# Kernel tuning notes

Hardware: AMD Instinct MI355X
Metric: run time of the kernel (lower is better)

Reference implementation:

```python
import jax, jax.numpy as jnp
from jax import lax
import numpy as np

B, CIN, L = 16, 512, 1024
COUT, K = 1024, 5          # conv out channels (GLU halves to 512), kernel size
DW = 512                    # word_feat == attn_channels == img_conv channels
HW = 196                    # 14*14 image feature locations


def setup_inputs() -> dict:
    key = jax.random.key(0)
    ks = jax.random.split(key, 8)
    s = 0.02
    return {
        "x": jax.random.normal(ks[0], (B, CIN, L), jnp.float32),
        "word_embed": jax.random.normal(ks[1], (B, L, DW), jnp.float32),
        "img_conv": jax.random.normal(ks[2], (B, DW, 14, 14), jnp.float32),
        "prev_attn": jnp.zeros((B, L, HW), jnp.float32),  # passed through, unused
        "conv_v": jax.random.normal(ks[3], (COUT, CIN, K), jnp.float32) * s,
        "conv_g": jnp.ones((COUT,), jnp.float32),
        "conv_b": jnp.zeros((COUT,), jnp.float32),
        "fc1_w": jax.random.normal(ks[4], (DW, DW), jnp.float32) * s,
        "fc1_b": jnp.zeros((DW,), jnp.float32),
        "fc2_w": jax.random.normal(ks[5], (DW, DW), jnp.float32) * s,
        "fc2_b": jnp.zeros((DW,), jnp.float32),
    }


def reference(x, word_embed, img_conv, prev_attn,
              conv_v, conv_g, conv_b, fc1_w, fc1_b, fc2_w, fc2_b):
    k = conv_v.shape[-1]
    # weight norm (PyTorch default dim=0): w = g * v / ||v||_{(in,k)}
    v_norm = jnp.sqrt(jnp.sum(conv_v * conv_v, axis=(1, 2), keepdims=True))
    w = (conv_g[:, None, None] / v_norm) * conv_v
    # Conv1d, padding=k-1 on both sides -> length L + k - 1 after ConvS2S trim
    y = lax.conv_general_dilated(x, w, window_strides=(1,),
                                 padding=[(k - 1, k - 1)],
                                 dimension_numbers=("NCH", "OIH", "NCH"))
    y = y + conv_b[None, :, None]
    # dropout is identity in eval mode
    a, b = jnp.split(y, 2, axis=1)          # GLU over channel dim
    h = a * jax.nn.sigmoid(b)
    h = h[:, :, : -(k - 1)]                  # [B, DW, L]
    identity_attn = h
    # attn_fc1 on [B, L, DW] then add word embeddings
    q = jnp.einsum("bcl,ac->bla", h, fc1_w) + fc1_b + word_embed  # [B, L, DW]
    feat = img_conv.reshape(img_conv.shape[0], img_conv.shape[1], -1)  # [B, DW, HW]
    score = jnp.einsum("bla,bap->blp", q, feat)   # [B, L, HW]
    attn = jax.nn.softmax(score, axis=-1)         # softmax over image locations
    ctx = jnp.einsum("blp,bap->bla", attn, feat)  # [B, L, DW]
    o = jnp.einsum("bla,ca->blc", ctx, fc2_w) + fc2_b
    out = o.transpose(0, 2, 1) + identity_attn
    # identity.shape == out.shape (input_feat == output_feat/2) -> no downsample
    out = out + x
    return (out, word_embed, img_conv, attn)
```

## Files before the change

### kernel.cpp

```cpp
#include <hip/hip_runtime.h>
#include <math.h>

#define NB   16
#define NCIN 512
#define NL   1024
#define NCOUT 1024
#define NK   5
#define NDW  512
#define NHW  196
#define NP   208
#define NPK  224

typedef unsigned short ushort_t;
typedef unsigned int uint_t;
typedef __attribute__((ext_vector_type(8))) short bf16x8;
typedef __attribute__((ext_vector_type(4))) float f32x4;

static __device__ __forceinline__ ushort_t f2bf(float f) {
  uint_t u = __builtin_bit_cast(uint_t, f);
  u += 0x7fff + ((u >> 16) & 1);
  return (ushort_t)(u >> 16);
}
static __device__ __forceinline__ float bf2f(ushort_t u) {
  uint_t v = ((uint_t)u) << 16;
  return __builtin_bit_cast(float, v);
}

__global__ __launch_bounds__(256) void wnorm_kernel(
    const float* __restrict__ v, const float* __restrict__ g,
    ushort_t* __restrict__ wperm) {
  const int o = blockIdx.x;
  const float* vr = v + (size_t)o * (NCIN * NK);
  float s = 0.f;
  for (int j = threadIdx.x; j < NCIN * NK; j += 256) {
    float t = vr[j];
    s += t * t;
  }
  for (int off = 32; off; off >>= 1) s += __shfl_down(s, off, 64);
  __shared__ float red[4];
  __shared__ float scale_s;
  const int wid = threadIdx.x >> 6;
  if ((threadIdx.x & 63) == 0) red[wid] = s;
  __syncthreads();
  if (threadIdx.x == 0) {
    float tot = red[0] + red[1] + red[2] + red[3];
    scale_s = g[o] / sqrtf(tot);
  }
  __syncthreads();
  const float scale = scale_s;
#pragma unroll
  for (int dk = 0; dk < NK; ++dk) {
    for (int ci = threadIdx.x; ci < NCIN; ci += 256) {
      wperm[((size_t)dk * NCOUT + o) * NCIN + ci] = f2bf(vr[ci * NK + dk] * scale);
    }
  }
}

__global__ __launch_bounds__(256) void xpose_kernel(
    const float* __restrict__ x, ushort_t* __restrict__ xT) {
  const int b = blockIdx.z;
  const int ci0 = blockIdx.y * 64;
  const int l0 = blockIdx.x * 64;
  const int tid = threadIdx.x;
  __shared__ float t[64][65];
  const float* xb = x + ((size_t)b * NCIN + ci0) * NL + l0;
#pragma unroll
  for (int r = 0; r < 4; ++r) {
    int row = r * 16 + (tid >> 4);
    int col = (tid & 15) * 4;
    float4 v = *(const float4*)&xb[(size_t)row * NL + col];
    t[row][col + 0] = v.x; t[row][col + 1] = v.y;
    t[row][col + 2] = v.z; t[row][col + 3] = v.w;
  }
  __syncthreads();
  ushort_t* xo = xT + ((size_t)b * NL + l0) * NCIN + ci0;
#pragma unroll
  for (int r = 0; r < 4; ++r) {
    int lrow = r * 16 + (tid >> 4);
    int cic = (tid & 15) * 4;
    ushort4 o4;
    o4.x = f2bf(t[cic + 0][lrow]);
    o4.y = f2bf(t[cic + 1][lrow]);
    o4.z = f2bf(t[cic + 2][lrow]);
    o4.w = f2bf(t[cic + 3][lrow]);
    *(ushort4*)&xo[(size_t)lrow * NCIN + cic] = o4;
  }
}

__global__ __launch_bounds__(256) void wcvt_kernel(
    const float* __restrict__ w1, const float* __restrict__ w2,
    ushort_t* __restrict__ w1bf, ushort_t* __restrict__ w2bf) {
  const int i = (blockIdx.x * 256 + threadIdx.x) * 4;
  {
    float4 v = *(const float4*)&w1[i];
    ushort4 o; o.x = f2bf(v.x); o.y = f2bf(v.y); o.z = f2bf(v.z); o.w = f2bf(v.w);
    *(ushort4*)&w1bf[i] = o;
  }
  {
    float4 v = *(const float4*)&w2[i];
    ushort4 o; o.x = f2bf(v.x); o.y = f2bf(v.y); o.z = f2bf(v.z); o.w = f2bf(v.w);
    *(ushort4*)&w2bf[i] = o;
  }
}

__global__ __launch_bounds__(256) void ftrans_kernel(
    const float* __restrict__ feat, ushort_t* __restrict__ fThi,
    ushort_t* __restrict__ fTlo, ushort_t* __restrict__ fbf) {
  const int b = blockIdx.y;
  const int a0 = blockIdx.x * 64;
  const int tid = threadIdx.x;
  __shared__ float t[64][200];

  const float* fb_ = feat + ((size_t)b * NDW + a0) * NHW;
#pragma unroll
  for (int pp = 0; pp < 16; ++pp) {
    int row = pp * 4 + (tid >> 6);
#pragma unroll
    for (int cc = 0; cc < 4; ++cc) {
      int col = cc * 64 + (tid & 63);
      if (col < NHW) t[row][col] = fb_[(size_t)row * NHW + col];
    }
  }
  __syncthreads();

  for (int pp = 0; pp < 13; ++pp) {
    int p = pp * 16 + (tid >> 4);
    int j = (tid & 15) * 4;
    ushort4 hi4, lo4;
#pragma unroll
    for (int k = 0; k < 4; ++k) {
      float v = (p < NHW) ? t[j + k][p] : 0.f;
      ushort_t h = f2bf(v);
      float lof = v - bf2f(h);
      ushort_t l = f2bf(lof);
      ((ushort_t*)&hi4)[k] = h;
      ((ushort_t*)&lo4)[k] = l;
    }
    size_t base = ((size_t)b * NP + p) * NDW + a0 + j;
    *(ushort4*)&fThi[base] = hi4;
    *(ushort4*)&fTlo[base] = lo4;
  }

#pragma unroll
  for (int cc = 0; cc < 4; ++cc) {
    int col = cc * 64 + (tid & 63);
    if (col < NPK) {
#pragma unroll
      for (int rr = 0; rr < 16; ++rr) {
        int al = rr * 4 + (tid >> 6);
        float v = (col < NHW) ? t[al][col] : 0.f;
        fbf[((size_t)b * NDW + a0 + al) * NPK + col] = f2bf(v);
      }
    }
  }
}

__global__ __launch_bounds__(256, 2) void conv_glu_mfma(
    const ushort_t* __restrict__ xT, const ushort_t* __restrict__ wperm,
    const float* __restrict__ conv_b, ushort_t* __restrict__ hbfT) {
  const int b  = blockIdx.z;
  const int c0 = blockIdx.y * 128;
  const int l0 = blockIdx.x * 128;
  const int tid = threadIdx.x;
  const int wid = tid >> 6;
  const int lane = tid & 63;
  const int wl = wid & 1;
  const int wc = wid >> 1;
  const int quad = lane >> 4;
  const int l16 = lane & 15;

  __shared__ ushort_t lx[128][72];
  __shared__ ushort_t lw[256][72];

  f32x4 accA[4][4], accB[4][4];
#pragma unroll
  for (int mt = 0; mt < 4; ++mt)
#pragma unroll
    for (int nt = 0; nt < 4; ++nt) {
      accA[mt][nt] = (f32x4){0.f, 0.f, 0.f, 0.f};
      accB[mt][nt] = (f32x4){0.f, 0.f, 0.f, 0.f};
    }

  const ushort_t* xTb = xT + (size_t)b * NL * NCIN;

  for (int dk = 0; dk < NK; ++dk) {
    const int lbase = l0 + dk - 4;
    const ushort_t* wpb = wperm + (size_t)dk * NCOUT * NCIN;
    for (int ci0 = 0; ci0 < NCIN; ci0 += 64) {
      __syncthreads();
#pragma unroll
      for (int it = 0; it < 4; ++it) {
        int t = tid + it * 256;
        int r = t >> 3, seg = t & 7;
        int gl = lbase + r;
        uint4 v = make_uint4(0u, 0u, 0u, 0u);
        if (gl >= 0)
          v = *(const uint4*)(xTb + (size_t)gl * NCIN + ci0 + seg * 8);
        *(uint4*)&lx[r][seg * 8] = v;
      }
#pragma unroll
      for (int it = 0; it < 8; ++it) {
        int t = tid + it * 256;
        int r = t >> 3, seg = t & 7;
        int co = (it < 4) ? (c0 + r) : (384 + c0 + r);
        uint4 v = *(const uint4*)(wpb + (size_t)co * NCIN + ci0 + seg * 8);
        *(uint4*)&lw[r][seg * 8] = v;
      }
      __syncthreads();
#pragma unroll
      for (int ks = 0; ks < 2; ++ks) {
        bf16x8 af[4];
#pragma unroll
        for (int mt = 0; mt < 4; ++mt)
          af[mt] = *(const bf16x8*)&lx[wl * 64 + mt * 16 + l16][ks * 32 + quad * 8];
#pragma unroll
        for (int nt = 0; nt < 4; ++nt) {
          bf16x8 bfa = *(const bf16x8*)&lw[wc * 64 + nt * 16 + l16][ks * 32 + quad * 8];
          bf16x8 bfb = *(const bf16x8*)&lw[128 + wc * 64 + nt * 16 + l16][ks * 32 + quad * 8];
#pragma unroll
          for (int mt = 0; mt < 4; ++mt) {
            accA[mt][nt] = __builtin_amdgcn_mfma_f32_16x16x32_bf16(af[mt], bfa, accA[mt][nt], 0, 0, 0);
            accB[mt][nt] = __builtin_amdgcn_mfma_f32_16x16x32_bf16(af[mt], bfb, accB[mt][nt], 0, 0, 0);
          }
        }
      }
    }
  }

#pragma unroll
  for (int nt = 0; nt < 4; ++nt) {
    const int co = c0 + wc * 64 + nt * 16 + l16;
    const float ba = conv_b[co];
    const float bb = conv_b[co + 512];
#pragma unroll
    for (int mt = 0; mt < 4; ++mt) {
      const int l = l0 + wl * 64 + mt * 16 + quad * 4;
      f32x4 a4 = accA[mt][nt];
      f32x4 b4 = accB[mt][nt];
#pragma unroll
      for (int r = 0; r < 4; ++r) {
        float aa = a4[r] + ba, bg = b4[r] + bb;
        float hv = aa * (1.f / (1.f + __expf(-bg)));
        hbfT[((size_t)b * NL + l + r) * NDW + co] = f2bf(hv);
      }
    }
  }
}

__global__ __launch_bounds__(256, 2) void fc1_mfma(
    const ushort_t* __restrict__ hbfT, const ushort_t* __restrict__ w1bf,
    const float* __restrict__ fb, const float* __restrict__ we,
    ushort_t* __restrict__ qhi, ushort_t* __restrict__ qlo) {
  const int b  = blockIdx.z;
  const int a0 = blockIdx.y * 128;
  const int l0 = blockIdx.x * 128;
  const int tid = threadIdx.x;
  const int wid = tid >> 6;
  const int lane = tid & 63;
  const int wl = wid & 1;
  const int wc = wid >> 1;
  const int quad = lane >> 4;
  const int l16 = lane & 15;

  __shared__ ushort_t la[128][72];
  __shared__ ushort_t lb[128][72];

  f32x4 acc[4][4];
#pragma unroll
  for (int mt = 0; mt < 4; ++mt)
#pragma unroll
    for (int nt = 0; nt < 4; ++nt) acc[mt][nt] = (f32x4){0.f, 0.f, 0.f, 0.f};

  const ushort_t* hb = hbfT + (size_t)b * NL * NDW;

  for (int c0 = 0; c0 < NDW; c0 += 64) {
    __syncthreads();
#pragma unroll
    for (int it = 0; it < 4; ++it) {
      int t = tid + it * 256;
      int r = t >> 3, seg = t & 7;
      *(uint4*)&la[r][seg * 8] = *(const uint4*)(hb + (size_t)(l0 + r) * NDW + c0 + seg * 8);
    }
#pragma unroll
    for (int it = 0; it < 4; ++it) {
      int t = tid + it * 256;
      int r = t >> 3, seg = t & 7;
      *(uint4*)&lb[r][seg * 8] = *(const uint4*)(w1bf + (size_t)(a0 + r) * NDW + c0 + seg * 8);
    }
    __syncthreads();
#pragma unroll
    for (int ks = 0; ks < 2; ++ks) {
      bf16x8 af[4];
#pragma unroll
      for (int mt = 0; mt < 4; ++mt)
        af[mt] = *(const bf16x8*)&la[wl * 64 + mt * 16 + l16][ks * 32 + quad * 8];
#pragma unroll
      for (int nt = 0; nt < 4; ++nt) {
        bf16x8 bf = *(const bf16x8*)&lb[wc * 64 + nt * 16 + l16][ks * 32 + quad * 8];
#pragma unroll
        for (int mt = 0; mt < 4; ++mt)
          acc[mt][nt] = __builtin_amdgcn_mfma_f32_16x16x32_bf16(af[mt], bf, acc[mt][nt], 0, 0, 0);
      }
    }
  }

#pragma unroll
  for (int nt = 0; nt < 4; ++nt) {
    const int a = a0 + wc * 64 + nt * 16 + l16;
    const float bias = fb[a];
#pragma unroll
    for (int mt = 0; mt < 4; ++mt) {
      const int l = l0 + wl * 64 + mt * 16 + quad * 4;
#pragma unroll
      for (int r = 0; r < 4; ++r) {
        size_t idx = ((size_t)b * NL + l + r) * NDW + a;
        float qv = acc[mt][nt][r] + bias + we[idx];
        ushort_t h = f2bf(qv);
        float lof = qv - bf2f(h);
        qhi[idx] = h;
        qlo[idx] = f2bf(lof);
      }
    }
  }
}

__global__ __launch_bounds__(256) void score_softmax(
    const ushort_t* __restrict__ qhi, const ushort_t* __restrict__ qlo,
    const ushort_t* __restrict__ fThi, const ushort_t* __restrict__ fTlo,
    float* __restrict__ out_attn) {
  const int b  = blockIdx.y;
  const int l0 = blockIdx.x * 64;
  const int tid = threadIdx.x;
  const int wid = tid >> 6;
  const int lane = tid & 63;
  const int quad = lane >> 4;
  const int l16 = lane & 15;

  __shared__ ushort_t qh[64][36], ql[64][36];
  __shared__ ushort_t fh[208][36], fl[208][36];

  f32x4 acc[13];
#pragma unroll
  for (int nt = 0; nt < 13; ++nt) acc[nt] = (f32x4){0.f, 0.f, 0.f, 0.f};

  for (int kc = 0; kc < 16; ++kc) {
    const int a0 = kc * 32;
    __syncthreads();
    {
      int r = tid >> 2, seg = tid & 3;
      size_t src = ((size_t)b * NL + l0 + r) * NDW + a0 + seg * 8;
      *(uint4*)&qh[r][seg * 8] = *(const uint4*)(qhi + src);
      *(uint4*)&ql[r][seg * 8] = *(const uint4*)(qlo + src);
#pragma unroll
      for (int it = 0; it < 4; ++it) {
        int row = it * 64 + (tid >> 2);
        if (row < NP) {
          size_t fsrc = ((size_t)b * NP + row) * NDW + a0 + seg * 8;
          *(uint4*)&fh[row][seg * 8] = *(const uint4*)(fThi + fsrc);
          *(uint4*)&fl[row][seg * 8] = *(const uint4*)(fTlo + fsrc);
        }
      }
    }
    __syncthreads();
    bf16x8 ah = *(const bf16x8*)&qh[wid * 16 + l16][quad * 8];
    bf16x8 al = *(const bf16x8*)&ql[wid * 16 + l16][quad * 8];
#pragma unroll
    for (int nt = 0; nt < 13; ++nt) {
      bf16x8 bh = *(const bf16x8*)&fh[nt * 16 + l16][quad * 8];
      bf16x8 bl = *(const bf16x8*)&fl[nt * 16 + l16][quad * 8];
      acc[nt] = __builtin_amdgcn_mfma_f32_16x16x32_bf16(ah, bh, acc[nt], 0, 0, 0);
      acc[nt] = __builtin_amdgcn_mfma_f32_16x16x32_bf16(al, bh, acc[nt], 0, 0, 0);
      acc[nt] = __builtin_amdgcn_mfma_f32_16x16x32_bf16(ah, bl, acc[nt], 0, 0, 0);
    }
  }

  const bool v12 = (l16 < 4);
#pragma unroll
  for (int r = 0; r < 4; ++r) {
    float mx = -1e30f;
#pragma unroll
    for (int nt = 0; nt < 12; ++nt) mx = fmaxf(mx, acc[nt][r]);
    if (v12) mx = fmaxf(mx, acc[12][r]);
#pragma unroll
    for (int off = 1; off < 16; off <<= 1) mx = fmaxf(mx, __shfl_xor(mx, off, 16));
    float ex[13];
    float sum = 0.f;
#pragma unroll
    for (int nt = 0; nt < 12; ++nt) { ex[nt] = __expf(acc[nt][r] - mx); sum += ex[nt]; }
    ex[12] = v12 ? __expf(acc[12][r] - mx) : 0.f;
    sum += ex[12];
#pragma unroll
    for (int off = 1; off < 16; off <<= 1) sum += __shfl_xor(sum, off, 16);
    const float inv = 1.f / sum;
    const int l = l0 + wid * 16 + quad * 4 + r;
    float* ao = out_attn + ((size_t)b * NL + l) * NHW;
#pragma unroll
    for (int nt = 0; nt < 13; ++nt) {
      int p = nt * 16 + l16;
      if (p < NHW) ao[p] = ex[nt] * inv;
    }
  }
}

__global__ __launch_bounds__(256, 2) void ctx_mfma(
    const float* __restrict__ attn, const ushort_t* __restrict__ fbf,
    ushort_t* __restrict__ ctx_bf) {
  const int b  = blockIdx.z;
  const int a0 = blockIdx.y * 128;
  const int l0 = blockIdx.x * 128;
  const int tid = threadIdx.x;
  const int wid = tid >> 6;
  const int lane = tid & 63;
  const int wl = wid & 1;
  const int wc = wid >> 1;
  const int quad = lane >> 4;
  const int l16 = lane & 15;

  __shared__ ushort_t la[128][36];
  __shared__ ushort_t lb[128][36];

  f32x4 acc[4][4];
#pragma unroll
  for (int mt = 0; mt < 4; ++mt)
#pragma unroll
    for (int nt = 0; nt < 4; ++nt) acc[mt][nt] = (f32x4){0.f, 0.f, 0.f, 0.f};

  for (int kc = 0; kc < 7; ++kc) {
    const int p0 = kc * 32;
    __syncthreads();
#pragma unroll
    for (int it = 0; it < 2; ++it) {
      int r = it * 64 + (tid >> 2), seg = tid & 3;
      int pb = p0 + seg * 8;
      const float* src = attn + ((size_t)b * NL + l0 + r) * NHW + pb;
      ushort4 o[2];
      if (pb + 7 < NHW) {
        float4 v0 = *(const float4*)src;
        float4 v1 = *(const float4*)(src + 4);
        o[0].x = f2bf(v0.x); o[0].y = f2bf(v0.y); o[0].z = f2bf(v0.z); o[0].w = f2bf(v0.w);
        o[1].x = f2bf(v1.x); o[1].y = f2bf(v1.y); o[1].z = f2bf(v1.z); o[1].w = f2bf(v1.w);
      } else {
#pragma unroll
        for (int k = 0; k < 8; ++k) {
          float v = (pb + k < NHW) ? src[k] : 0.f;
          ((ushort_t*)o)[k] = f2bf(v);
        }
      }
      *(uint4*)&la[r][seg * 8] = *(uint4*)o;
      const ushort_t* fsrc = fbf + ((size_t)b * NDW + a0 + r) * NPK + pb;
      *(uint4*)&lb[r][seg * 8] = *(const uint4*)fsrc;
    }
    __syncthreads();
    bf16x8 af[4];
#pragma unroll
    for (int mt = 0; mt < 4; ++mt)
      af[mt] = *(const bf16x8*)&la[wl * 64 + mt * 16 + l16][quad * 8];
#pragma unroll
    for (int nt = 0; nt < 4; ++nt) {
      bf16x8 bf = *(const bf16x8*)&lb[wc * 64 + nt * 16 + l16][quad * 8];
#pragma unroll
      for (int mt = 0; mt < 4; ++mt)
        acc[mt][nt] = __builtin_amdgcn_mfma_f32_16x16x32_bf16(af[mt], bf, acc[mt][nt], 0, 0, 0);
    }
  }

#pragma unroll
  for (int nt = 0; nt < 4; ++nt) {
    const int a = a0 + wc * 64 + nt * 16 + l16;
#pragma unroll
    for (int mt = 0; mt < 4; ++mt) {
      const int l = l0 + wl * 64 + mt * 16 + quad * 4;
#pragma unroll
      for (int r = 0; r < 4; ++r)
        ctx_bf[((size_t)b * NL + l + r) * NDW + a] = f2bf(acc[mt][nt][r]);
    }
  }
}

__global__ __launch_bounds__(256, 2) void fc2_mfma(
    const ushort_t* __restrict__ w2bf, const ushort_t* __restrict__ ctx_bf,
    const float* __restrict__ fb2, const ushort_t* __restrict__ hbfT,
    const float* __restrict__ x, float* __restrict__ out0) {
  const int b  = blockIdx.z;
  const int c0 = blockIdx.y * 128;
  const int l0 = blockIdx.x * 128;
  const int tid = threadIdx.x;
  const int wid = tid >> 6;
  const int lane = tid & 63;
  const int wl = wid & 1;
  const int wc = wid >> 1;
  const int quad = lane >> 4;
  const int l16 = lane & 15;

  __shared__ ushort_t la[128][72];
  __shared__ ushort_t lb[128][72];

  f32x4 acc[4][4];
#pragma unroll
  for (int mt = 0; mt < 4; ++mt)
#pragma unroll
    for (int nt = 0; nt < 4; ++nt) acc[mt][nt] = (f32x4){0.f, 0.f, 0.f, 0.f};

  for (int a0 = 0; a0 < NDW; a0 += 64) {
    __syncthreads();
#pragma unroll
    for (int it = 0; it < 4; ++it) {
      int t = tid + it * 256;
      int r = t >> 3, seg = t & 7;
      *(uint4*)&la[r][seg * 8] = *(const uint4*)(w2bf + (size_t)(c0 + r) * NDW + a0 + seg * 8);
    }
#pragma unroll
    for (int it = 0; it < 4; ++it) {
      int t = tid + it * 256;
      int r = t >> 3, seg = t & 7;
      *(uint4*)&lb[r][seg * 8] =
          *(const uint4*)(ctx_bf + ((size_t)b * NL + l0 + r) * NDW + a0 + seg * 8);
    }
    __syncthreads();
#pragma unroll
    for (int ks = 0; ks < 2; ++ks) {
      bf16x8 af[4];
#pragma unroll
      for (int mt = 0; mt < 4; ++mt)
        af[mt] = *(const bf16x8*)&la[wl * 64 + mt * 16 + l16][ks * 32 + quad * 8];
#pragma unroll
      for (int nt = 0; nt < 4; ++nt) {
        bf16x8 bf = *(const bf16x8*)&lb[wc * 64 + nt * 16 + l16][ks * 32 + quad * 8];
#pragma unroll
        for (int mt = 0; mt < 4; ++mt)
          acc[mt][nt] = __builtin_amdgcn_mfma_f32_16x16x32_bf16(af[mt], bf, acc[mt][nt], 0, 0, 0);
      }
    }
  }

#pragma unroll
  for (int mt = 0; mt < 4; ++mt) {
    const int cb = c0 + wl * 64 + mt * 16 + quad * 4;
    float4 bias4 = *(const float4*)&fb2[cb];
#pragma unroll
    for (int nt = 0; nt < 4; ++nt) {
      const int l = l0 + wc * 64 + nt * 16 + l16;
      ushort4 h4 = *(const ushort4*)&hbfT[((size_t)b * NL + l) * NDW + cb];
      const float bias[4] = {bias4.x, bias4.y, bias4.z, bias4.w};
      const ushort_t hs[4] = {h4.x, h4.y, h4.z, h4.w};
#pragma unroll
      for (int r = 0; r < 4; ++r) {
        size_t idx = ((size_t)b * NDW + cb + r) * NL + l;
        out0[idx] = acc[mt][nt][r] + bias[r] + bf2f(hs[r]) + x[idx];
      }
    }
  }
}

extern "C" void kernel_launch(void* const* d_in, const int* in_sizes, int n_in,
                              void* d_out, int out_size, void* d_ws, size_t ws_size,
                              hipStream_t stream) {
  const float* x      = (const float*)d_in[0];
  const float* we     = (const float*)d_in[1];
  const float* img    = (const float*)d_in[2];
  const float* conv_v = (const float*)d_in[4];
  const float* conv_g = (const float*)d_in[5];
  const float* conv_b = (const float*)d_in[6];
  const float* fc1_w  = (const float*)d_in[7];
  const float* fc1_b  = (const float*)d_in[8];
  const float* fc2_w  = (const float*)d_in[9];
  const float* fc2_b  = (const float*)d_in[10];

  float* out0     = (float*)d_out;
  float* out_we   = out0 + 8388608;
  float* out_img  = out_we + 8388608;
  float* out_attn = out_img + 1605632;

  ushort_t* wsu = (ushort_t*)d_ws;
  ushort_t* qhi   = wsu;
  ushort_t* qlo   = wsu + 8388608;
  ushort_t* wperm = wsu;
  ushort_t* xT    = wsu + 2621440;
  ushort_t* ctx_b = wsu;
  ushort_t* hbfT  = wsu + 16777216;
  ushort_t* w1bf  = wsu + 25165824;
  ushort_t* w2bf  = wsu + 25428968 - 263144 + 262144 + 144;
  w2bf = wsu + 25165824 + 262144;
  ushort_t* fThi  = wsu + 25690112;
  ushort_t* fTlo  = wsu + 27394048;
  ushort_t* fbf   = wsu + 29097984;

  wnorm_kernel<<<dim3(NCOUT), 256, 0, stream>>>(conv_v, conv_g, wperm);
  xpose_kernel<<<dim3(16, 8, NB), 256, 0, stream>>>(x, xT);
  wcvt_kernel<<<dim3(256), 256, 0, stream>>>(fc1_w, fc2_w, w1bf, w2bf);
  ftrans_kernel<<<dim3(8, NB), 256, 0, stream>>>(img, fThi, fTlo, fbf);

  conv_glu_mfma<<<dim3(8, 4, NB), 256, 0, stream>>>(xT, wperm, conv_b, hbfT);
  fc1_mfma<<<dim3(8, 4, NB), 256, 0, stream>>>(hbfT, w1bf, fc1_b, we, qhi, qlo);
  score_softmax<<<dim3(16, NB), 256, 0, stream>>>(qhi, qlo, fThi, fTlo, out_attn);
  ctx_mfma<<<dim3(8, 4, NB), 256, 0, stream>>>(out_attn, fbf, ctx_b);
  fc2_mfma<<<dim3(8, 4, NB), 256, 0, stream>>>(w2bf, ctx_b, fc2_b, hbfT, x, out0);

  hipMemcpyAsync(out_we, we, (size_t)8388608 * sizeof(float),
                 hipMemcpyDeviceToDevice, stream);
  hipMemcpyAsync(out_img, img, (size_t)1605632 * sizeof(float),
                 hipMemcpyDeviceToDevice, stream);
}
```

Baseline: 430.1 us.

## Rewrite conv GLU GEMM with double-buffered direct-to-LDS loads and larger tiles

The conv+GLU GEMM now uses 512-thread blocks with 256x256 tiles, double-buffered shared memory filled by global_load_lds, XOR-swizzled LDS layout and interleaved MFMA phases with setprio. The input transpose writes a zero-padded layout (NLG=1028 rows), which removes the boundary check. The conv weights are permuted so that the A and gate channels sit in the same tile. The goal is to overlap global loads with MFMA work and raise data reuse, at the cost of more LDS and registers and some hand-managed waitcnt and barrier logic.

Measured after the change: 410.4 us. 4.6% less time.

```diff
diff --git a/kernel.cpp b/kernel.cpp
--- a/kernel.cpp
+++ b/kernel.cpp
@@ -10,6 +10,7 @@
 #define NHW  196
 #define NP   208
 #define NPK  224
+#define NLG  1028
 
 typedef unsigned short ushort_t;
 typedef unsigned int uint_t;
@@ -24,6 +25,16 @@
 static __device__ __forceinline__ float bf2f(ushort_t u) {
   uint_t v = ((uint_t)u) << 16;
   return __builtin_bit_cast(float, v);
+}
+
+#define BARM()    asm volatile("s_barrier" ::: "memory")
+#define WAITVM8() asm volatile("s_waitcnt vmcnt(8)" ::: "memory")
+#define WAITVM0() asm volatile("s_waitcnt vmcnt(0)" ::: "memory")
+
+static __device__ __forceinline__ void gld16(const ushort_t* g, ushort_t* l) {
+  __builtin_amdgcn_global_load_lds(
+      (const __attribute__((address_space(1))) unsigned int*)g,
+      (__attribute__((address_space(3))) unsigned int*)l, 16, 0, 0);
 }
 
 __global__ __launch_bounds__(256) void wnorm_kernel(
@@ -48,10 +59,13 @@
   }
   __syncthreads();
   const float scale = scale_s;
+  const int isB = (o >= NDW) ? 1 : 0;
+  const int c = o - isB * NDW;
+  const int j = (c >> 5) * 64 + isB * 32 + (c & 31);
 #pragma unroll
   for (int dk = 0; dk < NK; ++dk) {
     for (int ci = threadIdx.x; ci < NCIN; ci += 256) {
-      wperm[((size_t)dk * NCOUT + o) * NCIN + ci] = f2bf(vr[ci * NK + dk] * scale);
+      wperm[((size_t)dk * NCOUT + j) * NCIN + ci] = f2bf(vr[ci * NK + dk] * scale);
     }
   }
 }
@@ -73,7 +87,7 @@
     t[row][col + 2] = v.z; t[row][col + 3] = v.w;
   }
   __syncthreads();
-  ushort_t* xo = xT + ((size_t)b * NL + l0) * NCIN + ci0;
+  ushort_t* xo = xT + ((size_t)b * NLG + l0 + 4) * NCIN + ci0;
 #pragma unroll
   for (int r = 0; r < 4; ++r) {
     int lrow = r * 16 + (tid >> 4);
@@ -85,6 +99,12 @@
     o4.w = f2bf(t[cic + 3][lrow]);
     *(ushort4*)&xo[(size_t)lrow * NCIN + cic] = o4;
   }
+  if (blockIdx.x == 0) {
+    for (int i = tid; i < 4 * 64; i += 256) {
+      int rr = i >> 6, cc = i & 63;
+      xT[((size_t)b * NLG + rr) * NCIN + ci0 + cc] = 0;
+    }
+  }
 }
 
 __global__ __launch_bounds__(256) void wcvt_kernel(
@@ -155,93 +175,155 @@
   }
 }
 
-__global__ __launch_bounds__(256, 2) void conv_glu_mfma(
+__global__ __launch_bounds__(512, 2) void conv_glu_mfma(
     const ushort_t* __restrict__ xT, const ushort_t* __restrict__ wperm,
     const float* __restrict__ conv_b, ushort_t* __restrict__ hbfT) {
-  const int b  = blockIdx.z;
-  const int c0 = blockIdx.y * 128;
-  const int l0 = blockIdx.x * 128;
+  const int bb = blockIdx.x >> 2;
+  const int l0 = (blockIdx.x & 3) * 256;
+  const int by = blockIdx.y;
   const int tid = threadIdx.x;
   const int wid = tid >> 6;
   const int lane = tid & 63;
-  const int wl = wid & 1;
-  const int wc = wid >> 1;
+  const int wm = wid >> 2;
+  const int wn = wid & 3;
   const int quad = lane >> 4;
   const int l16 = lane & 15;
-
-  __shared__ ushort_t lx[128][72];
-  __shared__ ushort_t lw[256][72];
-
-  f32x4 accA[4][4], accB[4][4];
-#pragma unroll
-  for (int mt = 0; mt < 4; ++mt)
-#pragma unroll
-    for (int nt = 0; nt < 4; ++nt) {
-      accA[mt][nt] = (f32x4){0.f, 0.f, 0.f, 0.f};
-      accB[mt][nt] = (f32x4){0.f, 0.f, 0.f, 0.f};
-    }
-
-  const ushort_t* xTb = xT + (size_t)b * NL * NCIN;
-
-  for (int dk = 0; dk < NK; ++dk) {
-    const int lbase = l0 + dk - 4;
-    const ushort_t* wpb = wperm + (size_t)dk * NCOUT * NCIN;
-    for (int ci0 = 0; ci0 < NCIN; ci0 += 64) {
-      __syncthreads();
-#pragma unroll
-      for (int it = 0; it < 4; ++it) {
-        int t = tid + it * 256;
-        int r = t >> 3, seg = t & 7;
-        int gl = lbase + r;
-        uint4 v = make_uint4(0u, 0u, 0u, 0u);
-        if (gl >= 0)
-          v = *(const uint4*)(xTb + (size_t)gl * NCIN + ci0 + seg * 8);
-        *(uint4*)&lx[r][seg * 8] = v;
-      }
-#pragma unroll
-      for (int it = 0; it < 8; ++it) {
-        int t = tid + it * 256;
-        int r = t >> 3, seg = t & 7;
-        int co = (it < 4) ? (c0 + r) : (384 + c0 + r);
-        uint4 v = *(const uint4*)(wpb + (size_t)co * NCIN + ci0 + seg * 8);
-        *(uint4*)&lw[r][seg * 8] = v;
-      }
-      __syncthreads();
-#pragma unroll
-      for (int ks = 0; ks < 2; ++ks) {
-        bf16x8 af[4];
+  const int sw = (l16 & 7) << 3;
+  const int csrc = ((lane & 7) ^ (lane >> 3)) << 3;
+
+  __shared__ ushort_t sA[2][256][64];
+  __shared__ ushort_t sB[2][256][64];
+
+  f32x4 acc[8][4];
+#pragma unroll
+  for (int mt = 0; mt < 8; ++mt)
+#pragma unroll
+    for (int nt = 0; nt < 4; ++nt) acc[mt][nt] = (f32x4){0.f, 0.f, 0.f, 0.f};
+
+  const ushort_t* gAbase = xT + (size_t)(bb * NLG + l0) * NCIN;
+  const int r0 = wid * 8 + (lane >> 3);
+  ushort_t* lA0 = &sA[0][0][0] + (wid * 64 + lane) * 8;
+  ushort_t* lB0 = &sB[0][0][0] + (wid * 64 + lane) * 8;
+
+  auto stage = [&](int tt, int s) {
+    const int dk = tt >> 3;
+    const int ci0 = (tt & 7) << 6;
+    const ushort_t* gA = gAbase + (size_t)dk * NCIN + ci0 + csrc;
+    const ushort_t* gB = wperm + ((size_t)dk * NCOUT + by * 256) * NCIN + ci0 + csrc;
+    ushort_t* lA = lA0 + s * (256 * 64);
+    ushort_t* lB = lB0 + s * (256 * 64);
+#pragma unroll
+    for (int c = 0; c < 4; ++c) {
+      gld16(gA + (size_t)(r0 + c * 64) * NCIN, lA + c * 4096);
+      gld16(gB + (size_t)(r0 + c * 64) * NCIN, lB + c * 4096);
+    }
+  };
+
+  stage(0, 0);
+  stage(1, 1);
+  WAITVM8();
+  BARM();
+
+  for (int t = 0; t < 40; ++t) {
+    const int s = t & 1;
+    bf16x8 af[4][2], bfr[4][2];
+
+#pragma unroll
+    for (int mt = 0; mt < 4; ++mt)
+#pragma unroll
+      for (int ks = 0; ks < 2; ++ks)
+        af[mt][ks] = *(const bf16x8*)&sA[s][wm * 128 + mt * 16 + l16]
+                                        [(ks * 32 + quad * 8) ^ sw];
+#pragma unroll
+    for (int nt = 0; nt < 2; ++nt)
+#pragma unroll
+      for (int ks = 0; ks < 2; ++ks)
+        bfr[nt][ks] = *(const bf16x8*)&sB[s][wn * 64 + nt * 16 + l16]
+                                         [(ks * 32 + quad * 8) ^ sw];
+    BARM();
+    __builtin_amdgcn_s_setprio(1);
+#pragma unroll
+    for (int ks = 0; ks < 2; ++ks)
+#pragma unroll
+      for (int nt = 0; nt < 2; ++nt)
 #pragma unroll
         for (int mt = 0; mt < 4; ++mt)
-          af[mt] = *(const bf16x8*)&lx[wl * 64 + mt * 16 + l16][ks * 32 + quad * 8];
-#pragma unroll
-        for (int nt = 0; nt < 4; ++nt) {
-          bf16x8 bfa = *(const bf16x8*)&lw[wc * 64 + nt * 16 + l16][ks * 32 + quad * 8];
-          bf16x8 bfb = *(const bf16x8*)&lw[128 + wc * 64 + nt * 16 + l16][ks * 32 + quad * 8];
-#pragma unroll
-          for (int mt = 0; mt < 4; ++mt) {
-            accA[mt][nt] = __builtin_amdgcn_mfma_f32_16x16x32_bf16(af[mt], bfa, accA[mt][nt], 0, 0, 0);
-            accB[mt][nt] = __builtin_amdgcn_mfma_f32_16x16x32_bf16(af[mt], bfb, accB[mt][nt], 0, 0, 0);
-          }
-        }
-      }
-    }
-  }
-
-#pragma unroll
-  for (int nt = 0; nt < 4; ++nt) {
-    const int co = c0 + wc * 64 + nt * 16 + l16;
-    const float ba = conv_b[co];
-    const float bb = conv_b[co + 512];
-#pragma unroll
-    for (int mt = 0; mt < 4; ++mt) {
-      const int l = l0 + wl * 64 + mt * 16 + quad * 4;
-      f32x4 a4 = accA[mt][nt];
-      f32x4 b4 = accB[mt][nt];
+          acc[mt][nt] = __builtin_amdgcn_mfma_f32_16x16x32_bf16(
+              af[mt][ks], bfr[nt][ks], acc[mt][nt], 0, 0, 0);
+    __builtin_amdgcn_s_setprio(0);
+    BARM();
+
+#pragma unroll
+    for (int nt = 2; nt < 4; ++nt)
+#pragma unroll
+      for (int ks = 0; ks < 2; ++ks)
+        bfr[nt][ks] = *(const bf16x8*)&sB[s][wn * 64 + nt * 16 + l16]
+                                         [(ks * 32 + quad * 8) ^ sw];
+    BARM();
+    __builtin_amdgcn_s_setprio(1);
+#pragma unroll
+    for (int ks = 0; ks < 2; ++ks)
+#pragma unroll
+      for (int nt = 2; nt < 4; ++nt)
+#pragma unroll
+        for (int mt = 0; mt < 4; ++mt)
+          acc[mt][nt] = __builtin_amdgcn_mfma_f32_16x16x32_bf16(
+              af[mt][ks], bfr[nt][ks], acc[mt][nt], 0, 0, 0);
+    __builtin_amdgcn_s_setprio(0);
+    BARM();
+
+#pragma unroll
+    for (int mt = 0; mt < 4; ++mt)
+#pragma unroll
+      for (int ks = 0; ks < 2; ++ks)
+        af[mt][ks] = *(const bf16x8*)&sA[s][wm * 128 + (4 + mt) * 16 + l16]
+                                        [(ks * 32 + quad * 8) ^ sw];
+    BARM();
+    __builtin_amdgcn_s_setprio(1);
+#pragma unroll
+    for (int ks = 0; ks < 2; ++ks)
+#pragma unroll
+      for (int nt = 0; nt < 2; ++nt)
+#pragma unroll
+        for (int mt = 0; mt < 4; ++mt)
+          acc[4 + mt][nt] = __builtin_amdgcn_mfma_f32_16x16x32_bf16(
+              af[mt][ks], bfr[nt][ks], acc[4 + mt][nt], 0, 0, 0);
+    __builtin_amdgcn_s_setprio(0);
+    BARM();
+
+    if (t < 38) stage(t + 2, s);
+    __builtin_amdgcn_s_setprio(1);
+#pragma unroll
+    for (int ks = 0; ks < 2; ++ks)
+#pragma unroll
+      for (int nt = 2; nt < 4; ++nt)
+#pragma unroll
+        for (int mt = 0; mt < 4; ++mt)
+          acc[4 + mt][nt] = __builtin_amdgcn_mfma_f32_16x16x32_bf16(
+              af[mt][ks], bfr[nt][ks], acc[4 + mt][nt], 0, 0, 0);
+    __builtin_amdgcn_s_setprio(0);
+
+    if (t < 39) {
+      if (t < 38) { WAITVM8(); } else { WAITVM0(); }
+      BARM();
+    }
+  }
+
+#pragma unroll
+  for (int nt = 0; nt < 2; ++nt) {
+    const int c = by * 128 + wn * 32 + nt * 16 + l16;
+    const float ba = conv_b[c];
+    const float bg = conv_b[c + NDW];
+#pragma unroll
+    for (int mt = 0; mt < 8; ++mt) {
+      const int lg = l0 + wm * 128 + mt * 16 + quad * 4;
+      ushort_t* ho = hbfT + ((size_t)bb * NL + lg) * NDW + c;
 #pragma unroll
       for (int r = 0; r < 4; ++r) {
-        float aa = a4[r] + ba, bg = b4[r] + bb;
-        float hv = aa * (1.f / (1.f + __expf(-bg)));
-        hbfT[((size_t)b * NL + l + r) * NDW + co] = f2bf(hv);
+        float aa = acc[mt][nt][r] + ba;
+        float gg = acc[mt][nt + 2][r] + bg;
+        float hv = aa * (1.f / (1.f + __expf(-gg)));
+        ho[(size_t)r * NDW] = f2bf(hv);
       }
     }
   }
@@ -579,8 +661,7 @@
   ushort_t* ctx_b = wsu;
   ushort_t* hbfT  = wsu + 16777216;
   ushort_t* w1bf  = wsu + 25165824;
-  ushort_t* w2bf  = wsu + 25428968 - 263144 + 262144 + 144;
-  w2bf = wsu + 25165824 + 262144;
+  ushort_t* w2bf  = wsu + 25165824 + 262144;
   ushort_t* fThi  = wsu + 25690112;
   ushort_t* fTlo  = wsu + 27394048;
   ushort_t* fbf   = wsu + 29097984;
@@ -590,7 +671,7 @@
   wcvt_kernel<<<dim3(256), 256, 0, stream>>>(fc1_w, fc2_w, w1bf, w2bf);
   ftrans_kernel<<<dim3(8, NB), 256, 0, stream>>>(img, fThi, fTlo, fbf);
 
-  conv_glu_mfma<<<dim3(8, 4, NB), 256, 0, stream>>>(xT, wperm, conv_b, hbfT);
+  conv_glu_mfma<<<dim3(64, 4), 512, 0, stream>>>(xT, wperm, conv_b, hbfT);
   fc1_mfma<<<dim3(8, 4, NB), 256, 0, stream>>>(hbfT, w1bf, fc1_b, we, qhi, qlo);
   score_softmax<<<dim3(16, NB), 256, 0, stream>>>(qhi, qlo, fThi, fTlo, out_attn);
   ctx_mfma<<<dim3(8, 4, NB), 256, 0, stream>>>(out_attn, fbf, ctx_b);
```
